# Kernel optimization log

Measured on AMD Instinct MI355X. Metric: run time of the kernel, lower is better.

The kernel has to match this reference:

```python
import jax, jax.numpy as jnp
import numpy as np

B, N, DIM = 4, 4096, 1024
HEADS, DIM_HEAD = 16, 64
DIM_INNER = HEADS * DIM_HEAD
ATTN_SCALE = 8.0
EPS = 1e-12  # F.normalize default eps


def setup_inputs() -> dict:
    key = jax.random.key(0)
    k1, k2, k3, k4, k5 = jax.random.split(key, 5)
    x = jax.random.normal(k1, (B, N, DIM), dtype=jnp.float32)
    gamma = jnp.ones((DIM,), dtype=jnp.float32)
    # stored as (in, out) so forward is x @ w
    w_qkv = jax.random.normal(k2, (DIM, 3 * DIM_INNER), dtype=jnp.float32) * (DIM ** -0.5)
    temperature = jnp.ones((HEADS, 1, 1), dtype=jnp.float32)
    w_out = jax.random.normal(k3, (DIM_INNER, DIM), dtype=jnp.float32) * (DIM_INNER ** -0.5)
    return {"x": x, "gamma": gamma, "w_qkv": w_qkv, "temperature": temperature, "w_out": w_out}


def _l2norm(t):
    # F.normalize(t, dim=-1): t / max(||t||_2, eps)
    n = jnp.linalg.norm(t, axis=-1, keepdims=True)
    return t / jnp.maximum(n, EPS)


def reference(x, gamma, w_qkv, temperature, w_out):
    b, n, dim = x.shape
    # RMSNorm: F.normalize(x, dim=-1) * sqrt(dim) * gamma
    xn = _l2norm(x) * (dim ** 0.5) * gamma
    # QKV projection -> qkv b h d n
    qkv = (xn @ w_qkv).reshape(b, n, 3, HEADS, DIM_HEAD)
    qkv = qkv.transpose(2, 0, 3, 4, 1)  # (3, b, h, d, n)
    q, k, v = qkv[0], qkv[1], qkv[2]
    # l2-normalize q, k over the sequence (last) axis; temperature-scale q
    q = _l2norm(q) * jnp.exp(temperature)  # temperature: (h,1,1) broadcast
    k = _l2norm(k)
    # cross-covariance attention over the small channel dim d
    sim = jnp.einsum('bhdn,bhen->bhde', q, k) * ATTN_SCALE
    attn = jax.nn.softmax(sim, axis=-1)
    out = jnp.einsum('bhde,bhen->bhdn', attn, v)
    # b h d n -> b n (h d), then out projection
    out = out.transpose(0, 3, 1, 2).reshape(b, n, DIM_INNER)
    return out @ w_out
```

## Files before the change

### kernel.cpp

```cpp
#include <hip/hip_runtime.h>
#include <stdint.h>

typedef unsigned short u16;
typedef unsigned int u32;
typedef __attribute__((ext_vector_type(8))) __bf16 bf16x8;
typedef __attribute__((ext_vector_type(4))) float f32x4;

#define M_TOT 16384
#define DIMX  1024

__device__ __forceinline__ u16 f2b(float f) {
  u32 u = __builtin_bit_cast(u32, f);
  u32 r = (u + 0x7fffu + ((u >> 16) & 1u)) >> 16;
  return (u16)r;
}

__device__ __forceinline__ void gl2lds16(const void* g, void* l) {
  __builtin_amdgcn_global_load_lds((const __attribute__((address_space(1))) void*)g,
                                   (__attribute__((address_space(3))) void*)l,
                                   16, 0, 0);
}

__global__ __launch_bounds__(256) void k_rms(const float* __restrict__ x,
                                             const float* __restrict__ gamma,
                                             u16* __restrict__ xn) {
  int row = blockIdx.x;
  int t = threadIdx.x;
  const float4* xr = (const float4*)(x + (size_t)row * DIMX);
  float4 v = xr[t];
  float ss = v.x * v.x + v.y * v.y + v.z * v.z + v.w * v.w;
#pragma unroll
  for (int o = 32; o > 0; o >>= 1) ss += __shfl_xor(ss, o, 64);
  __shared__ float wss[4];
  int w = t >> 6;
  if ((t & 63) == 0) wss[w] = ss;
  __syncthreads();
  float tot = wss[0] + wss[1] + wss[2] + wss[3];
  float scale = 32.0f / fmaxf(sqrtf(tot), 1e-12f);
  float4 g = ((const float4*)gamma)[t];
  ushort4 o4;
  o4.x = f2b(v.x * scale * g.x);
  o4.y = f2b(v.y * scale * g.y);
  o4.z = f2b(v.z * scale * g.z);
  o4.w = f2b(v.w * scale * g.w);
  ((ushort4*)xn)[(size_t)row * 256 + t] = o4;
}

__global__ __launch_bounds__(256) void k_castT(const float* __restrict__ in,
                                               u16* __restrict__ out, int Rr, int Cc) {
  __shared__ float tile[32][33];
  int c0 = blockIdx.x * 32, r0 = blockIdx.y * 32;
  int tx = threadIdx.x, ty = threadIdx.y;
#pragma unroll
  for (int i = 0; i < 4; i++)
    tile[ty + i * 8][tx] = in[(size_t)(r0 + ty + i * 8) * Cc + c0 + tx];
  __syncthreads();
#pragma unroll
  for (int i = 0; i < 4; i++)
    out[(size_t)(c0 + ty + i * 8) * Rr + r0 + tx] = f2b(tile[tx][ty + i * 8]);
}

template<bool SWAP>
__device__ __forceinline__ void gemm_core128(const u16* __restrict__ Ag,
                                             const u16* __restrict__ Bg,
                                             u16* Al, u16* Bl,
                                             int t, f32x4 (&acc)[4][4]) {
  int w = t >> 6, lane = t & 63;
  int r16 = lane & 15, q = lane >> 4;
  int wi = w >> 1, wj = w & 1;
  for (int k0 = 0; k0 < 1024; k0 += 64) {
    __syncthreads();
#pragma unroll
    for (int h = 0; h < 2; h++) {
#pragma unroll
      for (int r = 0; r < 2; r++) {
        int chunk = (r << 8) + t;
        int row = chunk >> 2, cc = chunk & 3;
        u16* la = Al + h * 4096 + ((r << 8) + (w << 6)) * 8;
        u16* lb = Bl + h * 4096 + ((r << 8) + (w << 6)) * 8;
        gl2lds16(Ag + (size_t)row * 1024 + k0 + h * 32 + cc * 8, la);
        gl2lds16(Bg + (size_t)row * 1024 + k0 + h * 32 + cc * 8, lb);
      }
    }
    __syncthreads();
#pragma unroll
    for (int h = 0; h < 2; h++) {
      bf16x8 af[4], bfr[4];
#pragma unroll
      for (int i = 0; i < 4; i++) {
        af[i]  = *(const bf16x8*)(Al + h * 4096 + (wi * 64 + i * 16 + r16) * 32 + q * 8);
        bfr[i] = *(const bf16x8*)(Bl + h * 4096 + (wj * 64 + i * 16 + r16) * 32 + q * 8);
      }
#pragma unroll
      for (int i = 0; i < 4; i++)
#pragma unroll
        for (int j = 0; j < 4; j++)
          acc[i][j] = SWAP
            ? __builtin_amdgcn_mfma_f32_16x16x32_bf16(bfr[j], af[i], acc[i][j], 0, 0, 0)
            : __builtin_amdgcn_mfma_f32_16x16x32_bf16(af[i], bfr[j], acc[i][j], 0, 0, 0);
    }
  }
}

__global__ __launch_bounds__(256) void k_gemm1qk(const u16* __restrict__ A,
                                                 const u16* __restrict__ Bt,
                                                 u16* __restrict__ qkT,
                                                 float* __restrict__ sumsq) {
  __shared__ u16 Al[2 * 4096];
  __shared__ u16 Bl[2 * 4096];
  int l = blockIdx.x;
  int xcd = l & 7, idx = l >> 3;
  int m0 = (xcd * 16 + (idx & 15)) * 128;
  int n0 = (idx >> 4) * 128;
  int t = threadIdx.x, lane = t & 63, w = t >> 6;
  int wi = w >> 1, wj = w & 1;
  int r16 = lane & 15, q = lane >> 4;
  f32x4 acc[4][4] = {};
  gemm_core128<false>(A + (size_t)m0 * 1024, Bt + (size_t)n0 * 1024, Al, Bl, t, acc);
  int b = m0 >> 12;
#pragma unroll
  for (int j = 0; j < 4; j++) {
    int c = n0 + wj * 64 + j * 16 + r16;
    float colss = 0.f;
#pragma unroll
    for (int i = 0; i < 4; i++) {
      f32x4 a = acc[i][j];
      colss += a.x * a.x + a.y * a.y + a.z * a.z + a.w * a.w;
      int m = m0 + wi * 64 + i * 16 + q * 4;
      ushort4 o4;
      o4.x = f2b(a.x); o4.y = f2b(a.y); o4.z = f2b(a.z); o4.w = f2b(a.w);
      *(ushort4*)(qkT + (size_t)c * M_TOT + m) = o4;
    }
    colss += __shfl_xor(colss, 16, 64);
    colss += __shfl_xor(colss, 32, 64);
    if (lane < 16) atomicAdd(&sumsq[b * 2048 + c], colss);
  }
}

__global__ __launch_bounds__(256) void k_gemm1v(const u16* __restrict__ A,
                                                const u16* __restrict__ BtV,
                                                u16* __restrict__ vmat) {
  __shared__ u16 Al[2 * 4096];
  __shared__ u16 Bl[2 * 4096];
  int l = blockIdx.x;
  int xcd = l & 7, idx = l >> 3;
  int m0 = (xcd * 16 + (idx & 15)) * 128;
  int vc0 = (idx >> 4) * 128;
  int t = threadIdx.x, lane = t & 63, w = t >> 6;
  int wi = w >> 1, wj = w & 1;
  int r16 = lane & 15, q = lane >> 4;
  f32x4 acc[4][4] = {};
  gemm_core128<true>(A + (size_t)m0 * 1024, BtV + (size_t)vc0 * 1024, Al, Bl, t, acc);
#pragma unroll
  for (int i = 0; i < 4; i++) {
    int m = m0 + wi * 64 + i * 16 + r16;
#pragma unroll
    for (int j = 0; j < 4; j++) {
      int c = vc0 + wj * 64 + j * 16 + q * 4;
      f32x4 a = acc[i][j];
      ushort4 o4;
      o4.x = f2b(a.x); o4.y = f2b(a.y); o4.z = f2b(a.z); o4.w = f2b(a.w);
      *(ushort4*)(vmat + (size_t)m * 1024 + c) = o4;
    }
  }
}

__global__ __launch_bounds__(256) void k_attn_s(const u16* __restrict__ qkT,
                                                float* __restrict__ S) {
  int bh = blockIdx.x, split = blockIdx.y;
  int b = bh >> 4, h = bh & 15;
  int t = threadIdx.x, lane = t & 63, w = t >> 6;
  int r16 = lane & 15, q = lane >> 4;
  const u16* qbase = qkT + (size_t)(h * 64) * M_TOT + b * 4096;
  const u16* kbase = qkT + (size_t)(1024 + h * 64) * M_TOT + b * 4096;
  f32x4 acc[4][4] = {};
#pragma unroll
  for (int it = 0; it < 4; it++) {
    int n0 = split * 512 + it * 128 + w * 32;
    int kk = n0 + q * 8;
    bf16x8 af[4], bfr[4];
#pragma unroll
    for (int i = 0; i < 4; i++) af[i] = *(const bf16x8*)(qbase + (size_t)(i * 16 + r16) * M_TOT + kk);
#pragma unroll
    for (int j = 0; j < 4; j++) bfr[j] = *(const bf16x8*)(kbase + (size_t)(j * 16 + r16) * M_TOT + kk);
#pragma unroll
    for (int i = 0; i < 4; i++)
#pragma unroll
      for (int j = 0; j < 4; j++)
        acc[i][j] = __builtin_amdgcn_mfma_f32_16x16x32_bf16(af[i], bfr[j], acc[i][j], 0, 0, 0);
  }
  float* Sb = S + (size_t)bh * 4096;
#pragma unroll
  for (int i = 0; i < 4; i++) {
    int d0 = i * 16 + q * 4;
#pragma unroll
    for (int j = 0; j < 4; j++) {
      int e = j * 16 + r16;
      atomicAdd(&Sb[(d0 + 0) * 64 + e], acc[i][j].x);
      atomicAdd(&Sb[(d0 + 1) * 64 + e], acc[i][j].y);
      atomicAdd(&Sb[(d0 + 2) * 64 + e], acc[i][j].z);
      atomicAdd(&Sb[(d0 + 3) * 64 + e], acc[i][j].w);
    }
  }
}

__global__ __launch_bounds__(64) void k_softmax(const float* __restrict__ S,
                                                const float* __restrict__ sumsq,
                                                const float* __restrict__ temp,
                                                u16* __restrict__ PT) {
  int bh = blockIdx.x;
  int b = bh >> 4, h = bh & 15;
  int d = threadIdx.x;
  __shared__ float rnk[64];
  rnk[d] = 1.0f / fmaxf(sqrtf(sumsq[b * 2048 + 1024 + h * 64 + d]), 1e-12f);
  __syncthreads();
  float nq = sqrtf(sumsq[b * 2048 + h * 64 + d]);
  float qs = 8.0f * __expf(temp[h]) / fmaxf(nq, 1e-12f);
  const float* Srow = S + ((size_t)bh * 64 + d) * 64;
  float vals[64];
  float mx = -3.0e38f;
#pragma unroll
  for (int e = 0; e < 64; e++) {
    float v = Srow[e] * qs * rnk[e];
    vals[e] = v;
    mx = fmaxf(mx, v);
  }
  float sum = 0.f;
#pragma unroll
  for (int e = 0; e < 64; e++) {
    float v = __expf(vals[e] - mx);
    vals[e] = v;
    sum += v;
  }
  float inv = 1.0f / sum;
#pragma unroll
  for (int e = 0; e < 64; e++)
    PT[((size_t)bh * 64 + e) * 64 + d] = f2b(vals[e] * inv);
}

__global__ __launch_bounds__(256) void k_m(const u16* __restrict__ woT,
                                           const u16* __restrict__ PT,
                                           u16* __restrict__ MT) {
  int bh = blockIdx.x;
  int b = bh >> 4, h = bh & 15;
  int o0 = blockIdx.y * 128;
  int t = threadIdx.x, lane = t & 63, w = t >> 6;
  int r16 = lane & 15, q = lane >> 4;
  const u16* pbase = PT + (size_t)bh * 4096;
  f32x4 acc[2][4] = {};
#pragma unroll
  for (int ks = 0; ks < 2; ks++) {
    int kk = ks * 32 + q * 8;
    bf16x8 af[2], bfr[4];
#pragma unroll
    for (int i = 0; i < 2; i++)
      af[i] = *(const bf16x8*)(woT + (size_t)(o0 + w * 32 + i * 16 + r16) * 1024 + h * 64 + kk);
#pragma unroll
    for (int j = 0; j < 4; j++)
      bfr[j] = *(const bf16x8*)(pbase + (size_t)(j * 16 + r16) * 64 + kk);
#pragma unroll
    for (int i = 0; i < 2; i++)
#pragma unroll
      for (int j = 0; j < 4; j++)
        acc[i][j] = __builtin_amdgcn_mfma_f32_16x16x32_bf16(af[i], bfr[j], acc[i][j], 0, 0, 0);
  }
  u16* dst = MT + (size_t)b * 1024 * 1024;
#pragma unroll
  for (int i = 0; i < 2; i++) {
    int o = o0 + w * 32 + i * 16 + q * 4;
#pragma unroll
    for (int j = 0; j < 4; j++) {
      int e = h * 64 + j * 16 + r16;
      f32x4 a = acc[i][j];
      dst[(size_t)(o + 0) * 1024 + e] = f2b(a.x);
      dst[(size_t)(o + 1) * 1024 + e] = f2b(a.y);
      dst[(size_t)(o + 2) * 1024 + e] = f2b(a.z);
      dst[(size_t)(o + 3) * 1024 + e] = f2b(a.w);
    }
  }
}

__global__ __launch_bounds__(256) void k_gemm2(const u16* __restrict__ A,
                                               const u16* __restrict__ Bt,
                                               float* __restrict__ C) {
  __shared__ u16 Al[2 * 4096];
  __shared__ u16 Bl[2 * 4096];
  int l = blockIdx.x;
  int xcd = l & 7, idx = l >> 3;
  int m0 = (xcd * 16 + (idx & 15)) * 128;
  int n0 = (idx >> 4) * 128;
  int b = m0 >> 12;
  const u16* Bb = Bt + (size_t)b * 1024 * 1024;
  int t = threadIdx.x, lane = t & 63, w = t >> 6;
  int wi = w >> 1, wj = w & 1;
  int r16 = lane & 15, q = lane >> 4;
  f32x4 acc[4][4] = {};
  gemm_core128<true>(A + (size_t)m0 * 1024, Bb + (size_t)n0 * 1024, Al, Bl, t, acc);
#pragma unroll
  for (int i = 0; i < 4; i++) {
    int m = m0 + wi * 64 + i * 16 + r16;
#pragma unroll
    for (int j = 0; j < 4; j++) {
      int c = n0 + wj * 64 + j * 16 + q * 4;
      *(f32x4*)(C + (size_t)m * 1024 + c) = acc[i][j];
    }
  }
}

extern "C" void kernel_launch(void* const* d_in, const int* in_sizes, int n_in,
                              void* d_out, int out_size, void* d_ws, size_t ws_size,
                              hipStream_t stream) {
  const float* x     = (const float*)d_in[0];
  const float* gamma = (const float*)d_in[1];
  const float* wqkv  = (const float*)d_in[2];
  const float* temp  = (const float*)d_in[3];
  const float* wout  = (const float*)d_in[4];
  float* out = (float*)d_out;

  char* ws = (char*)d_ws;
  size_t off = 0;
  u16* xn = (u16*)(ws + off);    off += (size_t)M_TOT * 1024 * 2;
  u16* wqT = (u16*)(ws + off);   off += (size_t)3072 * 1024 * 2;
  u16* woT = (u16*)(ws + off);   off += (size_t)1024 * 1024 * 2;
  u16* qkT = (u16*)(ws + off);   off += (size_t)2048 * M_TOT * 2;
  u16* vmat = (u16*)(ws + off);  off += (size_t)M_TOT * 1024 * 2;
  float* sumsq = (float*)(ws + off); off += (size_t)4 * 2048 * 4;
  float* S = (float*)(ws + off); off += (size_t)64 * 64 * 64 * 4;
  u16* PT = (u16*)(ws + off);    off += (size_t)64 * 64 * 64 * 2;
  u16* MT = (u16*)(ws + off);    off += (size_t)4 * 1024 * 1024 * 2;

  hipMemsetAsync((void*)sumsq, 0, (size_t)4 * 2048 * 4 + (size_t)64 * 64 * 64 * 4, stream);

  k_rms<<<16384, 256, 0, stream>>>(x, gamma, xn);
  dim3 cb(32, 8);
  k_castT<<<dim3(3072 / 32, 1024 / 32), cb, 0, stream>>>(wqkv, wqT, 1024, 3072);
  k_castT<<<dim3(1024 / 32, 1024 / 32), cb, 0, stream>>>(wout, woT, 1024, 1024);
  k_gemm1qk<<<2048, 256, 0, stream>>>(xn, wqT, qkT, sumsq);
  k_gemm1v<<<1024, 256, 0, stream>>>(xn, wqT + (size_t)2048 * 1024, vmat);
  k_attn_s<<<dim3(64, 8), 256, 0, stream>>>(qkT, S);
  k_softmax<<<64, 64, 0, stream>>>(S, sumsq, temp, PT);
  k_m<<<dim3(64, 8), 256, 0, stream>>>(woT, PT, MT);
  k_gemm2<<<1024, 256, 0, stream>>>(vmat, MT, out);
}
```

Before: 384.4 us.

## Swizzle LDS tiles in GEMM core and merge QK and V projection launches

Applies an XOR swizzle on the 16-byte column chunks of the LDS A/B tiles, both when async-loading from global and when reading MFMA fragments, to reduce LDS bank conflicts. Also fuses the separate QK and V projection GEMM kernels into one 3072-block launch that branches on the column tile. This removes one kernel launch and lets the V tail overlap with the QK tiles. The branch adds a little code size, and the swizzle changes the global load addressing pattern.

```diff
diff --git a/kernel.cpp b/kernel.cpp
--- a/kernel.cpp
+++ b/kernel.cpp
@@ -68,6 +68,8 @@
   int w = t >> 6, lane = t & 63;
   int r16 = lane & 15, q = lane >> 4;
   int wi = w >> 1, wj = w & 1;
+  int swz = (r16 >> 1) & 3;
+  int qs8 = ((q ^ swz) & 3) * 8;
   for (int k0 = 0; k0 < 1024; k0 += 64) {
     __syncthreads();
 #pragma unroll
@@ -75,7 +77,8 @@
 #pragma unroll
       for (int r = 0; r < 2; r++) {
         int chunk = (r << 8) + t;
-        int row = chunk >> 2, cc = chunk & 3;
+        int row = chunk >> 2;
+        int cc = (chunk & 3) ^ ((row >> 1) & 3);
         u16* la = Al + h * 4096 + ((r << 8) + (w << 6)) * 8;
         u16* lb = Bl + h * 4096 + ((r << 8) + (w << 6)) * 8;
         gl2lds16(Ag + (size_t)row * 1024 + k0 + h * 32 + cc * 8, la);
@@ -88,8 +91,8 @@
       bf16x8 af[4], bfr[4];
 #pragma unroll
       for (int i = 0; i < 4; i++) {
-        af[i]  = *(const bf16x8*)(Al + h * 4096 + (wi * 64 + i * 16 + r16) * 32 + q * 8);
-        bfr[i] = *(const bf16x8*)(Bl + h * 4096 + (wj * 64 + i * 16 + r16) * 32 + q * 8);
+        af[i]  = *(const bf16x8*)(Al + h * 4096 + (wi * 64 + i * 16 + r16) * 32 + qs8);
+        bfr[i] = *(const bf16x8*)(Bl + h * 4096 + (wj * 64 + i * 16 + r16) * 32 + qs8);
       }
 #pragma unroll
       for (int i = 0; i < 4; i++)
@@ -102,10 +105,11 @@
   }
 }
 
-__global__ __launch_bounds__(256) void k_gemm1qk(const u16* __restrict__ A,
-                                                 const u16* __restrict__ Bt,
-                                                 u16* __restrict__ qkT,
-                                                 float* __restrict__ sumsq) {
+__global__ __launch_bounds__(256) void k_gemm1(const u16* __restrict__ A,
+                                               const u16* __restrict__ Bt,
+                                               u16* __restrict__ qkT,
+                                               u16* __restrict__ vmat,
+                                               float* __restrict__ sumsq) {
   __shared__ u16 Al[2 * 4096];
   __shared__ u16 Bl[2 * 4096];
   int l = blockIdx.x;
@@ -116,51 +120,40 @@
   int wi = w >> 1, wj = w & 1;
   int r16 = lane & 15, q = lane >> 4;
   f32x4 acc[4][4] = {};
-  gemm_core128<false>(A + (size_t)m0 * 1024, Bt + (size_t)n0 * 1024, Al, Bl, t, acc);
-  int b = m0 >> 12;
-#pragma unroll
-  for (int j = 0; j < 4; j++) {
-    int c = n0 + wj * 64 + j * 16 + r16;
-    float colss = 0.f;
+  if (n0 < 2048) {
+    gemm_core128<false>(A + (size_t)m0 * 1024, Bt + (size_t)n0 * 1024, Al, Bl, t, acc);
+    int b = m0 >> 12;
+#pragma unroll
+    for (int j = 0; j < 4; j++) {
+      int c = n0 + wj * 64 + j * 16 + r16;
+      float colss = 0.f;
+#pragma unroll
+      for (int i = 0; i < 4; i++) {
+        f32x4 a = acc[i][j];
+        colss += a.x * a.x + a.y * a.y + a.z * a.z + a.w * a.w;
+        int m = m0 + wi * 64 + i * 16 + q * 4;
+        ushort4 o4;
+        o4.x = f2b(a.x); o4.y = f2b(a.y); o4.z = f2b(a.z); o4.w = f2b(a.w);
+        *(ushort4*)(qkT + (size_t)c * M_TOT + m) = o4;
+      }
+      colss += __shfl_xor(colss, 16, 64);
+      colss += __shfl_xor(colss, 32, 64);
+      if (lane < 16) atomicAdd(&sumsq[b * 2048 + c], colss);
+    }
+  } else {
+    gemm_core128<true>(A + (size_t)m0 * 1024, Bt + (size_t)n0 * 1024, Al, Bl, t, acc);
+    int vc0 = n0 - 2048;
 #pragma unroll
     for (int i = 0; i < 4; i++) {
-      f32x4 a = acc[i][j];
-      colss += a.x * a.x + a.y * a.y + a.z * a.z + a.w * a.w;
-      int m = m0 + wi * 64 + i * 16 + q * 4;
-      ushort4 o4;
-      o4.x = f2b(a.x); o4.y = f2b(a.y); o4.z = f2b(a.z); o4.w = f2b(a.w);
-      *(ushort4*)(qkT + (size_t)c * M_TOT + m) = o4;
-    }
-    colss += __shfl_xor(colss, 16, 64);
-    colss += __shfl_xor(colss, 32, 64);
-    if (lane < 16) atomicAdd(&sumsq[b * 2048 + c], colss);
-  }
-}
-
-__global__ __launch_bounds__(256) void k_gemm1v(const u16* __restrict__ A,
-                                                const u16* __restrict__ BtV,
-                                                u16* __restrict__ vmat) {
-  __shared__ u16 Al[2 * 4096];
-  __shared__ u16 Bl[2 * 4096];
-  int l = blockIdx.x;
-  int xcd = l & 7, idx = l >> 3;
-  int m0 = (xcd * 16 + (idx & 15)) * 128;
-  int vc0 = (idx >> 4) * 128;
-  int t = threadIdx.x, lane = t & 63, w = t >> 6;
-  int wi = w >> 1, wj = w & 1;
-  int r16 = lane & 15, q = lane >> 4;
-  f32x4 acc[4][4] = {};
-  gemm_core128<true>(A + (size_t)m0 * 1024, BtV + (size_t)vc0 * 1024, Al, Bl, t, acc);
-#pragma unroll
-  for (int i = 0; i < 4; i++) {
-    int m = m0 + wi * 64 + i * 16 + r16;
-#pragma unroll
-    for (int j = 0; j < 4; j++) {
-      int c = vc0 + wj * 64 + j * 16 + q * 4;
-      f32x4 a = acc[i][j];
-      ushort4 o4;
-      o4.x = f2b(a.x); o4.y = f2b(a.y); o4.z = f2b(a.z); o4.w = f2b(a.w);
-      *(ushort4*)(vmat + (size_t)m * 1024 + c) = o4;
+      int m = m0 + wi * 64 + i * 16 + r16;
+#pragma unroll
+      for (int j = 0; j < 4; j++) {
+        int c = vc0 + wj * 64 + j * 16 + q * 4;
+        f32x4 a = acc[i][j];
+        ushort4 o4;
+        o4.x = f2b(a.x); o4.y = f2b(a.y); o4.z = f2b(a.z); o4.w = f2b(a.w);
+        *(ushort4*)(vmat + (size_t)m * 1024 + c) = o4;
+      }
     }
   }
 }
@@ -335,8 +328,7 @@
   dim3 cb(32, 8);
   k_castT<<<dim3(3072 / 32, 1024 / 32), cb, 0, stream>>>(wqkv, wqT, 1024, 3072);
   k_castT<<<dim3(1024 / 32, 1024 / 32), cb, 0, stream>>>(wout, woT, 1024, 1024);
-  k_gemm1qk<<<2048, 256, 0, stream>>>(xn, wqT, qkT, sumsq);
-  k_gemm1v<<<1024, 256, 0, stream>>>(xn, wqT + (size_t)2048 * 1024, vmat);
+  k_gemm1<<<3072, 256, 0, stream>>>(xn, wqT, qkT, vmat, sumsq);
   k_attn_s<<<dim3(64, 8), 256, 0, stream>>>(qkT, S);
   k_softmax<<<64, 64, 0, stream>>>(S, sumsq, temp, PT);
   k_m<<<dim3(64, 8), 256, 0, stream>>>(woT, PT, MT);
```

Result: faster. 375.2 us (-2.4%).
